# Kernel optimization log

Hardware: AMD Instinct MI355X
Metric: run time of the kernel (lower is better)

The kernel has to match this reference:

```python
import jax, jax.numpy as jnp
import numpy as np

INPUT_DIM = 64
HIDDEN_DIM = 128
N_ROWS = 2_000_000
N_GROUPS = 2


def setup_inputs() -> dict:
    key = jax.random.key(0)
    k_x, k_T, k_w1, k_b1, k_w2, k_b2 = jax.random.split(key, 6)
    x = jax.random.normal(k_x, (N_ROWS, INPUT_DIM), dtype=jnp.float32)
    T = jax.random.randint(k_T, (N_ROWS,), 0, N_GROUPS, dtype=jnp.int64)
    # Linear params (torch convention: W @ x layout -> y = x @ W.T + b)
    lim1 = 1.0 / np.sqrt(INPUT_DIM)
    W1 = jax.random.uniform(k_w1, (HIDDEN_DIM, INPUT_DIM), jnp.float32, -lim1, lim1)
    b1 = jax.random.uniform(k_b1, (HIDDEN_DIM,), jnp.float32, -lim1, lim1)
    lim2 = 1.0 / np.sqrt(HIDDEN_DIM)
    W2 = jax.random.uniform(k_w2, (1, HIDDEN_DIM), jnp.float32, -lim2, lim2)
    b2 = jax.random.uniform(k_b2, (1,), jnp.float32, -lim2, lim2)
    return {"x": x, "T": T, "W1": W1, "b1": b1, "W2": W2, "b2": b2}


def reference(x, T, W1, b1, W2, b2):
    # s = f2(tanh(f1(x))).flatten()  -> [N]
    h = jnp.tanh(x @ W1.T + b1)                      # [N, H]
    s = (h @ W2.T + b2).reshape(-1)                  # [N]
    e = jnp.exp(s)                                   # faithful to torch.exp (unshifted)
    # group sums via segment_sum (2 groups), then gather-normalize per row
    sums = jax.ops.segment_sum(e, T, num_segments=N_GROUPS)  # [2]
    return e / sums[T]
```

## Files before the change

### kernel.cpp

```cpp
#include <hip/hip_runtime.h>
#include <math.h>

#define NROWS 2000000
#define IN_DIM 64
#define HID 128
#define NTILES (NROWS / 16)

typedef __bf16 bf16x8 __attribute__((ext_vector_type(8)));
typedef float f32x4 __attribute__((ext_vector_type(4)));

__device__ __forceinline__ float tanh_fast(float a) {
    float p = __expf(2.0f * a);
    float r = __builtin_amdgcn_rcpf(p + 1.0f);
    return fmaf(-2.0f, r, 1.0f);
}

__device__ __forceinline__ void split8(f32x4 a, f32x4 b, bf16x8& h, bf16x8& l) {
    #pragma unroll
    for (int j = 0; j < 4; j++) {
        __bf16 hb = (__bf16)a[j];
        h[j] = hb;
        l[j] = (__bf16)(a[j] - (float)hb);
    }
    #pragma unroll
    for (int j = 0; j < 4; j++) {
        __bf16 hb = (__bf16)b[j];
        h[4 + j] = hb;
        l[4 + j] = (__bf16)(b[j] - (float)hb);
    }
}

__global__ void zero_sums_kernel(float* g) {
    if (threadIdx.x < 2) g[threadIdx.x] = 0.0f;
}

__global__ __launch_bounds__(256, 2) void fused_mfma_kernel(
    const float* __restrict__ x, const int* __restrict__ T,
    const float* __restrict__ W1, const float* __restrict__ b1,
    const float* __restrict__ W2, const float* __restrict__ b2,
    float* __restrict__ e_out, float* __restrict__ gsums)
{
    const int lane = threadIdx.x & 63;
    const int c16  = lane & 15;
    const int g4   = lane >> 4;
    const int gwave = blockIdx.x * (blockDim.x >> 6) + (threadIdx.x >> 6);
    const int nwave = gridDim.x * (blockDim.x >> 6);

    int tile = gwave;
    f32x4 xq0, xq1, xq2, xq3;
    {
        const float* xp = x + (size_t)(tile * 16 + c16) * IN_DIM + g4 * 8;
        xq0 = *(const f32x4*)(xp);
        xq1 = *(const f32x4*)(xp + 4);
        xq2 = *(const f32x4*)(xp + 32);
        xq3 = *(const f32x4*)(xp + 36);
    }

    bf16x8 w1h[8][2], w1l[8][2];
    #pragma unroll
    for (int t = 0; t < 8; t++) {
        #pragma unroll
        for (int c = 0; c < 2; c++) {
            const float* wp = W1 + (size_t)(t * 16 + c16) * IN_DIM + c * 32 + g4 * 8;
            f32x4 a = *(const f32x4*)wp;
            f32x4 b = *(const f32x4*)(wp + 4);
            split8(a, b, w1h[t][c], w1l[t][c]);
        }
    }
    float b1v[8], w2v[8];
    #pragma unroll
    for (int t = 0; t < 8; t++) {
        b1v[t] = b1[t * 16 + c16];
        w2v[t] = W2[t * 16 + c16];
    }
    const float b2v = b2[0];

    float ls0 = 0.f, ls1 = 0.f;

    for (; tile < NTILES; tile += nwave) {
        bf16x8 xh0, xh1, xl0, xl1;
        split8(xq0, xq1, xh0, xl0);
        split8(xq2, xq3, xh1, xl1);

        int nt = tile + nwave;
        if (nt < NTILES) {
            const float* xp = x + (size_t)(nt * 16 + c16) * IN_DIM + g4 * 8;
            xq0 = *(const f32x4*)(xp);
            xq1 = *(const f32x4*)(xp + 4);
            xq2 = *(const f32x4*)(xp + 32);
            xq3 = *(const f32x4*)(xp + 36);
        }

        f32x4 acc[8];
        #pragma unroll
        for (int t = 0; t < 8; t++) acc[t] = (f32x4){0.f, 0.f, 0.f, 0.f};
        #pragma unroll
        for (int t = 0; t < 8; t++) {
            acc[t] = __builtin_amdgcn_mfma_f32_16x16x32_bf16(xh0, w1h[t][0], acc[t], 0, 0, 0);
            acc[t] = __builtin_amdgcn_mfma_f32_16x16x32_bf16(xl0, w1h[t][0], acc[t], 0, 0, 0);
            acc[t] = __builtin_amdgcn_mfma_f32_16x16x32_bf16(xh0, w1l[t][0], acc[t], 0, 0, 0);
            acc[t] = __builtin_amdgcn_mfma_f32_16x16x32_bf16(xl0, w1l[t][0], acc[t], 0, 0, 0);
            acc[t] = __builtin_amdgcn_mfma_f32_16x16x32_bf16(xh1, w1h[t][1], acc[t], 0, 0, 0);
            acc[t] = __builtin_amdgcn_mfma_f32_16x16x32_bf16(xl1, w1h[t][1], acc[t], 0, 0, 0);
            acc[t] = __builtin_amdgcn_mfma_f32_16x16x32_bf16(xh1, w1l[t][1], acc[t], 0, 0, 0);
            acc[t] = __builtin_amdgcn_mfma_f32_16x16x32_bf16(xl1, w1l[t][1], acc[t], 0, 0, 0);
        }

        float sp0 = 0.f, sp1 = 0.f, sp2 = 0.f, sp3 = 0.f;
        #pragma unroll
        for (int t = 0; t < 8; t++) {
            sp0 = fmaf(tanh_fast(acc[t][0] + b1v[t]), w2v[t], sp0);
            sp1 = fmaf(tanh_fast(acc[t][1] + b1v[t]), w2v[t], sp1);
            sp2 = fmaf(tanh_fast(acc[t][2] + b1v[t]), w2v[t], sp2);
            sp3 = fmaf(tanh_fast(acc[t][3] + b1v[t]), w2v[t], sp3);
        }
        #pragma unroll
        for (int m = 1; m < 16; m <<= 1) {
            sp0 += __shfl_xor(sp0, m, 16);
            sp1 += __shfl_xor(sp1, m, 16);
            sp2 += __shfl_xor(sp2, m, 16);
            sp3 += __shfl_xor(sp3, m, 16);
        }
        if (c16 < 4) {
            float sv = (c16 == 0) ? sp0 : (c16 == 1) ? sp1 : (c16 == 2) ? sp2 : sp3;
            float e = __expf(sv + b2v);
            int row = tile * 16 + g4 * 4 + c16;
            e_out[row] = e;
            if (T[row] == 0) ls0 += e; else ls1 += e;
        }
    }

    #pragma unroll
    for (int off = 32; off > 0; off >>= 1) {
        ls0 += __shfl_down(ls0, off, 64);
        ls1 += __shfl_down(ls1, off, 64);
    }
    if (lane == 0) {
        atomicAdd(&gsums[0], ls0);
        atomicAdd(&gsums[1], ls1);
    }
}

__global__ __launch_bounds__(256) void normalize_kernel(
    float* __restrict__ e_out, const int* __restrict__ T,
    const float* __restrict__ gsums)
{
    const float inv0 = 1.0f / gsums[0];
    const float inv1 = 1.0f / gsums[1];
    const int n4 = NROWS / 4;
    const int stride = gridDim.x * blockDim.x;
    for (int i = blockIdx.x * blockDim.x + threadIdx.x; i < n4; i += stride) {
        float4 e = reinterpret_cast<const float4*>(e_out)[i];
        int4  t = reinterpret_cast<const int4*>(T)[i];
        e.x *= (t.x == 0) ? inv0 : inv1;
        e.y *= (t.y == 0) ? inv0 : inv1;
        e.z *= (t.z == 0) ? inv0 : inv1;
        e.w *= (t.w == 0) ? inv0 : inv1;
        reinterpret_cast<float4*>(e_out)[i] = e;
    }
}

extern "C" void kernel_launch(void* const* d_in, const int* in_sizes, int n_in,
                              void* d_out, int out_size, void* d_ws, size_t ws_size,
                              hipStream_t stream) {
    const float* x  = (const float*)d_in[0];
    const int*   T  = (const int*)d_in[1];
    const float* W1 = (const float*)d_in[2];
    const float* b1 = (const float*)d_in[3];
    const float* W2 = (const float*)d_in[4];
    const float* b2 = (const float*)d_in[5];
    float* e_out = (float*)d_out;
    float* gsums = (float*)d_ws;

    zero_sums_kernel<<<1, 64, 0, stream>>>(gsums);

    fused_mfma_kernel<<<512, 256, 0, stream>>>(x, T, W1, b1, W2, b2, e_out, gsums);

    normalize_kernel<<<2048, 256, 0, stream>>>(e_out, T, gsums);
}
```

Measured before the change: 199.1 us.

## Stage x tiles through swizzled LDS, share split W1 in LDS, drop lo*lo MFMAs

Each wave now loads its 16-row x tile with fully coalesced contiguous f32x4 loads, stores it into a per-wave XOR-swizzled LDS buffer, and reads back the MFMA fragment layout from there. The hi/lo bf16 split of W1 is computed once per block into shared memory rather than held in registers by every wave. The lo*lo MFMA terms are dropped, cutting the product count from 8 to 6 per output tile. Block size grows to 512 with higher occupancy bounds. The cost is extra LDS traffic for both x and weights on every tile, and a small loss of precision in the split-bf16 emulation.

```diff
diff --git a/kernel.cpp b/kernel.cpp
--- a/kernel.cpp
+++ b/kernel.cpp
@@ -5,6 +5,9 @@
 #define IN_DIM 64
 #define HID 128
 #define NTILES (NROWS / 16)
+#define BLOCK 512
+#define NBLK 512
+#define WPB (BLOCK / 64)
 
 typedef __bf16 bf16x8 __attribute__((ext_vector_type(8)));
 typedef float f32x4 __attribute__((ext_vector_type(4)));
@@ -34,39 +37,40 @@
     if (threadIdx.x < 2) g[threadIdx.x] = 0.0f;
 }
 
-__global__ __launch_bounds__(256, 2) void fused_mfma_kernel(
+__global__ __launch_bounds__(BLOCK, 4) void fused_mfma_kernel(
     const float* __restrict__ x, const int* __restrict__ T,
     const float* __restrict__ W1, const float* __restrict__ b1,
     const float* __restrict__ W2, const float* __restrict__ b2,
     float* __restrict__ e_out, float* __restrict__ gsums)
 {
+    __shared__ __bf16 wlds[2][8][2][64][8];
+    __shared__ float xlds[WPB][1024];
+
     const int lane = threadIdx.x & 63;
+    const int wv   = threadIdx.x >> 6;
     const int c16  = lane & 15;
     const int g4   = lane >> 4;
-    const int gwave = blockIdx.x * (blockDim.x >> 6) + (threadIdx.x >> 6);
-    const int nwave = gridDim.x * (blockDim.x >> 6);
-
-    int tile = gwave;
-    f32x4 xq0, xq1, xq2, xq3;
+
     {
-        const float* xp = x + (size_t)(tile * 16 + c16) * IN_DIM + g4 * 8;
-        xq0 = *(const f32x4*)(xp);
-        xq1 = *(const f32x4*)(xp + 4);
-        xq2 = *(const f32x4*)(xp + 32);
-        xq3 = *(const f32x4*)(xp + 36);
-    }
-
-    bf16x8 w1h[8][2], w1l[8][2];
-    #pragma unroll
-    for (int t = 0; t < 8; t++) {
+        const int t = wv;
+        const int n = t * 16 + c16;
         #pragma unroll
         for (int c = 0; c < 2; c++) {
-            const float* wp = W1 + (size_t)(t * 16 + c16) * IN_DIM + c * 32 + g4 * 8;
-            f32x4 a = *(const f32x4*)wp;
-            f32x4 b = *(const f32x4*)(wp + 4);
-            split8(a, b, w1h[t][c], w1l[t][c]);
-        }
-    }
+            const int kb = c * 32 + g4 * 8;
+            bf16x8 h, l;
+            #pragma unroll
+            for (int j = 0; j < 8; j++) {
+                float w = W1[n * IN_DIM + kb + j];
+                __bf16 hb = (__bf16)w;
+                h[j] = hb;
+                l[j] = (__bf16)(w - (float)hb);
+            }
+            *(bf16x8*)&wlds[0][t][c][lane][0] = h;
+            *(bf16x8*)&wlds[1][t][c][lane][0] = l;
+        }
+    }
+    __syncthreads();
+
     float b1v[8], w2v[8];
     #pragma unroll
     for (int t = 0; t < 8; t++) {
@@ -75,35 +79,62 @@
     }
     const float b2v = b2[0];
 
+    float* xb = xlds[wv];
+    const int gwave = blockIdx.x * WPB + wv;
+    const int nwave = NBLK * WPB;
+
     float ls0 = 0.f, ls1 = 0.f;
 
+    int tile = gwave;
+    f32x4 g0, g1, g2, g3;
+    {
+        const float* xs = x + (size_t)tile * 1024 + lane * 4;
+        g0 = *(const f32x4*)(xs);
+        g1 = *(const f32x4*)(xs + 256);
+        g2 = *(const f32x4*)(xs + 512);
+        g3 = *(const f32x4*)(xs + 768);
+        const int l4 = lane * 4;
+        *(f32x4*)&xb[(0 * 256 + l4) ^ ((((0 * 256 + l4) >> 6) & 7) << 2)] = g0;
+        *(f32x4*)&xb[(1 * 256 + l4) ^ ((((1 * 256 + l4) >> 6) & 7) << 2)] = g1;
+        *(f32x4*)&xb[(2 * 256 + l4) ^ ((((2 * 256 + l4) >> 6) & 7) << 2)] = g2;
+        *(f32x4*)&xb[(3 * 256 + l4) ^ ((((3 * 256 + l4) >> 6) & 7) << 2)] = g3;
+    }
+
     for (; tile < NTILES; tile += nwave) {
-        bf16x8 xh0, xh1, xl0, xl1;
-        split8(xq0, xq1, xh0, xl0);
-        split8(xq2, xq3, xh1, xl1);
-
-        int nt = tile + nwave;
+        const int nt = tile + nwave;
         if (nt < NTILES) {
-            const float* xp = x + (size_t)(nt * 16 + c16) * IN_DIM + g4 * 8;
-            xq0 = *(const f32x4*)(xp);
-            xq1 = *(const f32x4*)(xp + 4);
-            xq2 = *(const f32x4*)(xp + 32);
-            xq3 = *(const f32x4*)(xp + 36);
-        }
+            const float* xs = x + (size_t)nt * 1024 + lane * 4;
+            g0 = *(const f32x4*)(xs);
+            g1 = *(const f32x4*)(xs + 256);
+            g2 = *(const f32x4*)(xs + 512);
+            g3 = *(const f32x4*)(xs + 768);
+        }
+
+        const int sw = (c16 & 7) << 2;
+        const int base = c16 * 64 + g4 * 8;
+        f32x4 a0 = *(const f32x4*)&xb[(base + 0)  ^ sw];
+        f32x4 a1 = *(const f32x4*)&xb[(base + 4)  ^ sw];
+        f32x4 a2 = *(const f32x4*)&xb[(base + 32) ^ sw];
+        f32x4 a3 = *(const f32x4*)&xb[(base + 36) ^ sw];
+        bf16x8 xh0, xl0, xh1, xl1;
+        split8(a0, a1, xh0, xl0);
+        split8(a2, a3, xh1, xl1);
 
         f32x4 acc[8];
         #pragma unroll
         for (int t = 0; t < 8; t++) acc[t] = (f32x4){0.f, 0.f, 0.f, 0.f};
         #pragma unroll
         for (int t = 0; t < 8; t++) {
-            acc[t] = __builtin_amdgcn_mfma_f32_16x16x32_bf16(xh0, w1h[t][0], acc[t], 0, 0, 0);
-            acc[t] = __builtin_amdgcn_mfma_f32_16x16x32_bf16(xl0, w1h[t][0], acc[t], 0, 0, 0);
-            acc[t] = __builtin_amdgcn_mfma_f32_16x16x32_bf16(xh0, w1l[t][0], acc[t], 0, 0, 0);
-            acc[t] = __builtin_amdgcn_mfma_f32_16x16x32_bf16(xl0, w1l[t][0], acc[t], 0, 0, 0);
-            acc[t] = __builtin_amdgcn_mfma_f32_16x16x32_bf16(xh1, w1h[t][1], acc[t], 0, 0, 0);
-            acc[t] = __builtin_amdgcn_mfma_f32_16x16x32_bf16(xl1, w1h[t][1], acc[t], 0, 0, 0);
-            acc[t] = __builtin_amdgcn_mfma_f32_16x16x32_bf16(xh1, w1l[t][1], acc[t], 0, 0, 0);
-            acc[t] = __builtin_amdgcn_mfma_f32_16x16x32_bf16(xl1, w1l[t][1], acc[t], 0, 0, 0);
+            bf16x8 wh0 = *(const bf16x8*)&wlds[0][t][0][lane][0];
+            bf16x8 wl0 = *(const bf16x8*)&wlds[1][t][0][lane][0];
+            bf16x8 wh1 = *(const bf16x8*)&wlds[0][t][1][lane][0];
+            bf16x8 wl1 = *(const bf16x8*)&wlds[1][t][1][lane][0];
+            acc[t] = __builtin_amdgcn_mfma_f32_16x16x32_bf16(xh0, wh0, acc[t], 0, 0, 0);
+            acc[t] = __builtin_amdgcn_mfma_f32_16x16x32_bf16(xl0, wh0, acc[t], 0, 0, 0);
+            acc[t] = __builtin_amdgcn_mfma_f32_16x16x32_bf16(xh0, wl0, acc[t], 0, 0, 0);
+            acc[t] = __builtin_amdgcn_mfma_f32_16x16x32_bf16(xh1, wh1, acc[t], 0, 0, 0);
+            acc[t] = __builtin_amdgcn_mfma_f32_16x16x32_bf16(xl1, wh1, acc[t], 0, 0, 0);
+            acc[t] = __builtin_amdgcn_mfma_f32_16x16x32_bf16(xh1, wl1, acc[t], 0, 0, 0);
         }
 
         float sp0 = 0.f, sp1 = 0.f, sp2 = 0.f, sp3 = 0.f;
@@ -122,11 +153,19 @@
             sp3 += __shfl_xor(sp3, m, 16);
         }
         if (c16 < 4) {
-            float sv = (c16 == 0) ? sp0 : (c16 == 1) ? sp1 : (c16 == 2) ? sp2 : sp3;
-            float e = __expf(sv + b2v);
+            float svv = (c16 == 0) ? sp0 : (c16 == 1) ? sp1 : (c16 == 2) ? sp2 : sp3;
+            float e = __expf(svv + b2v);
             int row = tile * 16 + g4 * 4 + c16;
             e_out[row] = e;
             if (T[row] == 0) ls0 += e; else ls1 += e;
+        }
+
+        if (nt < NTILES) {
+            const int l4 = lane * 4;
+            *(f32x4*)&xb[(0 * 256 + l4) ^ ((((0 * 256 + l4) >> 6) & 7) << 2)] = g0;
+            *(f32x4*)&xb[(1 * 256 + l4) ^ ((((1 * 256 + l4) >> 6) & 7) << 2)] = g1;
+            *(f32x4*)&xb[(2 * 256 + l4) ^ ((((2 * 256 + l4) >> 6) & 7) << 2)] = g2;
+            *(f32x4*)&xb[(3 * 256 + l4) ^ ((((3 * 256 + l4) >> 6) & 7) << 2)] = g3;
         }
     }
 
@@ -174,7 +213,7 @@
 
     zero_sums_kernel<<<1, 64, 0, stream>>>(gsums);
 
-    fused_mfma_kernel<<<512, 256, 0, stream>>>(x, T, W1, b1, W2, b2, e_out, gsums);
+    fused_mfma_kernel<<<NBLK, BLOCK, 0, stream>>>(x, T, W1, b1, W2, b2, e_out, gsums);
 
     normalize_kernel<<<2048, 256, 0, stream>>>(e_out, T, gsums);
 }
```

New measurement: 694.9 us. 3.49x slower.
